# Optimization experiments

Hardware: AMD Instinct MI355X
Metric: run time of the kernel (lower is better)

The kernel has to match this reference:

```python
import jax, jax.numpy as jnp
import numpy as np

H = 1.0  # primo_h
N_GRID = 768


def _grid_mesh(n):
    ii, jj = np.meshgrid(np.arange(n - 1), np.arange(n - 1), indexing='ij')
    v00 = (ii * n + jj).ravel(); v10 = ((ii + 1) * n + jj).ravel()
    v01 = (ii * n + jj + 1).ravel(); v11 = ((ii + 1) * n + jj + 1).ravel()
    tri1 = np.stack([v00, v10, v01], 1); tri2 = np.stack([v10, v11, v01], 1)
    return np.concatenate([tri1, tri2], 0).astype(np.int32)  # [F,3]


def _face_adjacency(faces):
    # faces: [F,3] -> edges [E,2] (sorted vertex pairs), face_ids [E,2]
    F = faces.shape[0]
    fe = np.stack([faces[:, [0, 1]], faces[:, [1, 2]], faces[:, [2, 0]]], 1).reshape(-1, 2)
    fe = np.sort(fe, axis=1)
    fid = np.repeat(np.arange(F, dtype=np.int32), 3)
    order = np.lexsort((fe[:, 1], fe[:, 0]))
    fs, fi = fe[order], fid[order]
    same = np.all(fs[:-1] == fs[1:], axis=1)
    k = np.nonzero(same)[0]
    edges = fs[k].astype(np.int32)
    face_ids = np.stack([fi[k], fi[k + 1]], 1).astype(np.int32)
    return edges, face_ids


def setup_inputs() -> dict:
    key = jax.random.key(0)
    k1, k2, k3 = jax.random.split(key, 3)
    faces_np = _grid_mesh(N_GRID)                      # [F,3]
    edges_np, face_ids_np = _face_adjacency(faces_np)  # [E,2],[E,2]
    F = faces_np.shape[0]
    V = N_GRID * N_GRID
    return {
        'transformed_prism': jax.random.normal(k1, (F, 3, 3), dtype=jnp.float32),
        'rotations': jax.random.normal(k2, (F, 3, 3), dtype=jnp.float32),
        'verts': jax.random.normal(k3, (1, V, 3), dtype=jnp.float32),
        'faces': jnp.asarray(faces_np.T),       # [3,F], matches torch forward arg
        'edges': jnp.asarray(edges_np),
        'face_ids': jnp.asarray(face_ids_np),
    }


def _verts_id_face(Ft, E, Q):
    # Ft: [F,3] faces; E: [e,2] edge vertex ids; Q: [e,2] adjacent face ids
    fa, fb = Ft[Q[:, 0]], Ft[Q[:, 1]]  # [e,3]

    def find(fv, tgt):
        return jnp.where(fv[:, 0] == tgt, 0,
               jnp.where(fv[:, 1] == tgt, 1,
               jnp.where(fv[:, 2] == tgt, 2, -1)))

    return jnp.stack([find(fa, E[:, 0]), find(fa, E[:, 1]),
                      find(fb, E[:, 0]), find(fb, E[:, 1])], axis=1)  # [e,4]


def reference(transformed_prism, rotations, verts, faces, edges, face_ids):
    tp = transformed_prism
    bs = verts.shape[0]
    v = verts.reshape(-1, 3)
    Ft = faces.T  # [F,3]

    # per-face normals (vectorized version of the original per-face loop)
    e1 = tp[:, 0] - tp[:, 1]
    e2 = tp[:, 0] - tp[:, 2]
    nrm = jnp.cross(e1, e2)
    normals = nrm / jnp.linalg.norm(nrm, axis=-1, keepdims=True)  # [F,3]

    # face areas
    p1, p2, p3 = v[Ft[:, 0]], v[Ft[:, 1]], v[Ft[:, 2]]
    face_areas = 0.5 * jnp.linalg.norm(jnp.cross(p2 - p1, p3 - p1), axis=1)

    # faithful to original: normals indexed by edge VERTEX ids
    n1, n2 = normals[edges[:, 0]], normals[edges[:, 1]]
    fid1, fid2 = face_ids[:, 0], face_ids[:, 1]
    r1, r2 = rotations[fid1], rotations[fid2]

    ftv = _verts_id_face(Ft, edges, face_ids)  # [e,4]
    v1_p1, v2_p1 = tp[fid1, ftv[:, 0]], tp[fid1, ftv[:, 1]]
    v1_p2, v2_p2 = tp[fid2, ftv[:, 2]], tp[fid2, ftv[:, 3]]

    p1n1 = jnp.einsum('ec,ecd->ed', n1, r1)
    p1n2 = jnp.einsum('ec,ecd->ed', n2, r1)
    p2n1 = jnp.einsum('ec,ecd->ed', n1, r2)
    p2n2 = jnp.einsum('ec,ecd->ed', n2, r2)

    A = jnp.stack([v1_p1 + p1n1 * H, v2_p1 + p1n2 * H,
                   v1_p1 - p1n1 * H, v2_p1 - p1n2 * H], axis=1)  # [e,4,3]
    B = jnp.stack([v1_p2 + p2n1 * H, v2_p2 + p2n2 * H,
                   v1_p2 - p2n1 * H, v2_p2 - p2n2 * H], axis=1)
    D = A - B

    # coeff[p,q] = 2^{-|i_p-i_q|-|j_p-j_q|}, (i,j) over {0,1}^2
    idx = jnp.array([[0, 0], [0, 1], [1, 0], [1, 1]], dtype=jnp.float32)
    coeff = 2.0 ** (-jnp.abs(idx[:, None] - idx[None, :]).sum(-1))  # [4,4]
    pair = jnp.einsum('epc,eqc->epq', D, D)
    energy = (pair * coeff).sum((1, 2)) / 9.0  # [e]

    weight = jnp.sum((v[edges[:, 0]] - v[edges[:, 1]]) ** 2, axis=1) \
             / (face_areas[fid1] + face_areas[fid2])
    return (energy * weight).sum() / bs
```

## Files before the change

kernel.cpp:

```cpp
#include <hip/hip_runtime.h>


struct __attribute__((aligned(4))) F4 { float a, b, c, d; };
struct __attribute__((aligned(4))) F3 { float x, y, z; };

__device__ __forceinline__ void load9(const float* __restrict__ p, float* d) {
    F4 u0 = *(const F4*)p;
    F4 u1 = *(const F4*)(p + 4);
    d[0] = u0.a; d[1] = u0.b; d[2] = u0.c; d[3] = u0.d;
    d[4] = u1.a; d[5] = u1.b; d[6] = u1.c; d[7] = u1.d;
    d[8] = p[8];
}

__device__ __forceinline__ void load6(const float* __restrict__ p, float* d) {
    F4 u = *(const F4*)p;
    d[0] = u.a; d[1] = u.b; d[2] = u.c; d[3] = u.d;
    d[4] = p[4]; d[5] = p[5];
}

__device__ __forceinline__ F3 load3(const float* __restrict__ p) {
    F3 r; r.x = p[0]; r.y = p[1]; r.z = p[2]; return r;
}

__device__ __forceinline__ float edge_ew(const float* u1, const float* u2,
                                         const float* w1, const float* w2,
                                         const float* rA, const float* rB,
                                         const F3& n1, const F3& n2,
                                         const F3& pa, const F3& pb,
                                         float asum) {
    float ux = u1[0] - u2[0], uy = u1[1] - u2[1], uz = u1[2] - u2[2];
    float wx = w1[0] - w2[0], wy = w1[1] - w2[1], wz = w1[2] - w2[2];

    float d0 = rA[0] - rB[0], d1 = rA[1] - rB[1], d2 = rA[2] - rB[2];
    float d3 = rA[3] - rB[3], d4 = rA[4] - rB[4], d5 = rA[5] - rB[5];
    float d6 = rA[6] - rB[6], d7 = rA[7] - rB[7], d8 = rA[8] - rB[8];

    float ax = n1.x * d0 + n1.y * d3 + n1.z * d6;
    float ay = n1.x * d1 + n1.y * d4 + n1.z * d7;
    float az = n1.x * d2 + n1.y * d5 + n1.z * d8;
    float bx = n2.x * d0 + n2.y * d3 + n2.z * d6;
    float by = n2.x * d1 + n2.y * d4 + n2.z * d7;
    float bz = n2.x * d2 + n2.y * d5 + n2.z * d8;

    float uu = ux * ux + uy * uy + uz * uz;
    float ww = wx * wx + wy * wy + wz * wz;
    float uw = ux * wx + uy * wy + uz * wz;
    float aa = ax * ax + ay * ay + az * az;
    float bb = bx * bx + by * by + bz * bz;
    float ab = ax * bx + ay * by + az * bz;
    float energy = (3.0f * (uu + ww + uw) + (aa + bb + ab)) * (1.0f / 9.0f);

    float dx = pa.x - pb.x, dy = pa.y - pb.y, dz = pa.z - pb.z;
    float weight = (dx * dx + dy * dy + dz * dz) / asum;
    return energy * weight;
}

__global__ void prep_kernel(const float* __restrict__ tp,
                            const float* __restrict__ verts,
                            float* __restrict__ normals,
                            float* __restrict__ areas,
                            double* __restrict__ acc,
                            int n, int V, int Q) {
    int t = blockIdx.x * blockDim.x + threadIdx.x;
    if (t == 0) *acc = 0.0;

    if (t < V) {
        float r[9];
        load9(tp + (size_t)9 * t, r);
        float e1x = r[0] - r[3], e1y = r[1] - r[4], e1z = r[2] - r[5];
        float e2x = r[0] - r[6], e2y = r[1] - r[7], e2z = r[2] - r[8];
        float nx = e1y * e2z - e1z * e2y;
        float ny = e1z * e2x - e1x * e2z;
        float nz = e1x * e2y - e1y * e2x;
        float inv = 1.0f / sqrtf(nx * nx + ny * ny + nz * nz);
        normals[3 * t]     = nx * inv;
        normals[3 * t + 1] = ny * inv;
        normals[3 * t + 2] = nz * inv;
    }

    if (t < Q) {
        int m = n - 1;
        int i = t / m;
        int j = t - i * m;
        int v00 = i * n + j;
        F3 p00 = load3(verts + (size_t)3 * v00);
        F3 p01 = load3(verts + (size_t)3 * (v00 + 1));
        F3 p10 = load3(verts + (size_t)3 * (v00 + n));
        F3 p11 = load3(verts + (size_t)3 * (v00 + n + 1));
        {
            float ax = p10.x - p00.x, ay = p10.y - p00.y, az = p10.z - p00.z;
            float bx = p01.x - p00.x, by = p01.y - p00.y, bz = p01.z - p00.z;
            float cx = ay * bz - az * by;
            float cy = az * bx - ax * bz;
            float cz = ax * by - ay * bx;
            areas[t] = 0.5f * sqrtf(cx * cx + cy * cy + cz * cz);
        }
        {
            float ax = p11.x - p10.x, ay = p11.y - p10.y, az = p11.z - p10.z;
            float bx = p01.x - p10.x, by = p01.y - p10.y, bz = p01.z - p10.z;
            float cx = ay * bz - az * by;
            float cy = az * bx - ax * bz;
            float cz = ax * by - ay * bx;
            areas[Q + t] = 0.5f * sqrtf(cx * cx + cy * cy + cz * cz);
        }
    }
}

__global__ void edge_kernel(const float* __restrict__ tp,
                            const float* __restrict__ rot,
                            const float* __restrict__ verts,
                            const float* __restrict__ normals,
                            const float* __restrict__ areas,
                            double* __restrict__ acc,
                            int n, int Q) {
    int q = blockIdx.x * blockDim.x + threadIdx.x;
    double term = 0.0;
    if (q < Q) {
        int m = n - 1;
        int i = q / m;
        int j = q - i * m;
        int v00 = i * n + j;
        int v01 = v00 + 1;
        int v10 = v00 + n;

        float t1[9], t2[9], r1[9], r2[9];
        load9(tp  + (size_t)9 * q, t1);
        load9(tp  + (size_t)9 * (Q + q), t2);
        load9(rot + (size_t)9 * q, r1);
        load9(rot + (size_t)9 * (Q + q), r2);
        float a1 = areas[q];
        float a2 = areas[Q + q];

        F3 nA = load3(normals + (size_t)3 * v00);
        F3 nB = load3(normals + (size_t)3 * v01);
        F3 nC = load3(normals + (size_t)3 * v10);
        F3 pA = load3(verts + (size_t)3 * v00);
        F3 pB = load3(verts + (size_t)3 * v01);
        F3 pC = load3(verts + (size_t)3 * v10);

        float sum = 0.0f;
        sum += edge_ew(t1 + 6, t2 + 6, t1 + 3, t2 + 0, r1, r2,
                       nB, nC, pB, pC, a1 + a2);
        if (i > 0) {
            int f2 = Q + q - m;
            float rh[9], th[6];
            load9(rot + (size_t)9 * f2, rh);
            load6(tp + (size_t)9 * f2, th);
            sum += edge_ew(t1 + 0, th + 0, t1 + 6, th + 3, r1, rh,
                           nA, nB, pA, pB, a1 + areas[f2]);
        }
        if (j > 0) {
            int f2 = Q + q - 1;
            float rv[9], tv[6];
            load9(rot + (size_t)9 * f2, rv);
            load6(tp + (size_t)9 * f2 + 3, tv);
            sum += edge_ew(t1 + 0, tv + 3, t1 + 3, tv + 0, r1, rv,
                           nA, nC, pA, pC, a1 + areas[f2]);
        }
        term = (double)sum;
    }

#pragma unroll
    for (int off = 32; off > 0; off >>= 1) term += __shfl_down(term, off, 64);
    __shared__ double sdata[4];
    int lane = threadIdx.x & 63;
    int wid = threadIdx.x >> 6;
    if (lane == 0) sdata[wid] = term;
    __syncthreads();
    if (threadIdx.x == 0) {
        double s = sdata[0] + sdata[1] + sdata[2] + sdata[3];
        atomicAdd(acc, s);
    }
}

__global__ void finalize_kernel(const double* __restrict__ acc,
                                float* __restrict__ out) {
    if (threadIdx.x == 0 && blockIdx.x == 0) out[0] = (float)(*acc);
}

extern "C" void kernel_launch(void* const* d_in, const int* in_sizes, int n_in,
                              void* d_out, int out_size, void* d_ws, size_t ws_size,
                              hipStream_t stream) {
    const float* tp    = (const float*)d_in[0];
    const float* rot   = (const float*)d_in[1];
    const float* verts = (const float*)d_in[2];

    int V = in_sizes[2] / 3;
    int n = (int)(sqrtf((float)V) + 0.5f);
    int Q = (n - 1) * (n - 1);

    double* acc     = (double*)d_ws;
    float*  normals = (float*)((char*)d_ws + 16);
    float*  areas   = normals + (size_t)3 * V;
    float*  out     = (float*)d_out;

    const int B = 256;
    int gp = (max(V, Q) + B - 1) / B;
    prep_kernel<<<gp, B, 0, stream>>>(tp, verts, normals, areas, acc, n, V, Q);
    int ge = (Q + B - 1) / B;
    edge_kernel<<<ge, B, 0, stream>>>(tp, rot, verts, normals, areas, acc, n, Q);
    finalize_kernel<<<1, 64, 0, stream>>>(acc, out);
}
```

Before: 170.9 us.

## Fuse prep and edge kernels into a 2D-tiled kernel with shared-memory halos

Replaces the separate normals/areas prep kernel and per-quad edge kernel with one 2D-tiled kernel. Each block stages its faces, neighbor faces, vertices and recomputed normals and areas in LDS, including halos, so the intermediate arrays are never written to or read back from global memory. The global double atomic is replaced by per-block partials summed in a final reduction kernel. In exchange, halo data is loaded and recomputed redundantly, the stride-9 element-wise loads into LDS may coalesce poorly, and the large LDS footprint (roughly 40 KB per block) limits occupancy.

```diff
diff --git a/kernel.cpp b/kernel.cpp
--- a/kernel.cpp
+++ b/kernel.cpp
@@ -1,25 +1,22 @@
 #include <hip/hip_runtime.h>
 
 
-struct __attribute__((aligned(4))) F4 { float a, b, c, d; };
-struct __attribute__((aligned(4))) F3 { float x, y, z; };
+#define TI 8
+#define TJ 32
+
+struct __attribute__((aligned(4))) F4s { float a, b, c, d; };
+struct F3 { float x, y, z; };
 
 __device__ __forceinline__ void load9(const float* __restrict__ p, float* d) {
-    F4 u0 = *(const F4*)p;
-    F4 u1 = *(const F4*)(p + 4);
+    F4s u0 = *(const F4s*)p;
+    F4s u1 = *(const F4s*)(p + 4);
     d[0] = u0.a; d[1] = u0.b; d[2] = u0.c; d[3] = u0.d;
     d[4] = u1.a; d[5] = u1.b; d[6] = u1.c; d[7] = u1.d;
     d[8] = p[8];
 }
 
-__device__ __forceinline__ void load6(const float* __restrict__ p, float* d) {
-    F4 u = *(const F4*)p;
-    d[0] = u.a; d[1] = u.b; d[2] = u.c; d[3] = u.d;
-    d[4] = p[4]; d[5] = p[5];
-}
-
-__device__ __forceinline__ F3 load3(const float* __restrict__ p) {
-    F3 r; r.x = p[0]; r.y = p[1]; r.z = p[2]; return r;
+__device__ __forceinline__ int iclamp(int x, int lo, int hi) {
+    return x < lo ? lo : (x > hi ? hi : x);
 }
 
 __device__ __forceinline__ float edge_ew(const float* u1, const float* u2,
@@ -51,131 +48,165 @@
     float energy = (3.0f * (uu + ww + uw) + (aa + bb + ab)) * (1.0f / 9.0f);
 
     float dx = pa.x - pb.x, dy = pa.y - pb.y, dz = pa.z - pb.z;
-    float weight = (dx * dx + dy * dy + dz * dz) / asum;
-    return energy * weight;
-}
-
-__global__ void prep_kernel(const float* __restrict__ tp,
-                            const float* __restrict__ verts,
-                            float* __restrict__ normals,
-                            float* __restrict__ areas,
-                            double* __restrict__ acc,
-                            int n, int V, int Q) {
-    int t = blockIdx.x * blockDim.x + threadIdx.x;
-    if (t == 0) *acc = 0.0;
-
-    if (t < V) {
+    return energy * (dx * dx + dy * dy + dz * dz) / asum;
+}
+
+__global__ __launch_bounds__(256) void fused_kernel(
+        const float* __restrict__ tp,
+        const float* __restrict__ rot,
+        const float* __restrict__ verts,
+        double* __restrict__ partials,
+        int n) {
+    const int m = n - 1;
+    const int Q = m * m;
+    const int tid = threadIdx.x;
+    const int i0 = blockIdx.y * TI;
+    const int j0 = blockIdx.x * TJ;
+
+    __shared__ float sT1[TI * TJ * 9];
+    __shared__ float sR1[TI * TJ * 9];
+    __shared__ float sT2[(TI + 1) * (TJ + 1) * 9];
+    __shared__ float sR2[(TI + 1) * (TJ + 1) * 9];
+    __shared__ float sV[(TI + 2) * (TJ + 2) * 3];
+    __shared__ float sN[(TI + 1) * (TJ + 1) * 3];
+    __shared__ float sA1[TI * TJ];
+    __shared__ float sA2[(TI + 1) * (TJ + 1)];
+    __shared__ double sred[4];
+
+    for (int idx = tid; idx < TI * TJ * 9; idx += 256) {
+        int r = idx / (TJ * 9);
+        int o = idx - r * (TJ * 9);
+        int k = o / 9, c = o - k * 9;
+        int gi = iclamp(i0 + r, 0, m - 1);
+        int gj = iclamp(j0 + k, 0, m - 1);
+        size_t f = (size_t)gi * m + gj;
+        sT1[idx] = tp[9 * f + c];
+        sR1[idx] = rot[9 * f + c];
+    }
+    for (int idx = tid; idx < (TI + 1) * (TJ + 1) * 9; idx += 256) {
+        int r = idx / ((TJ + 1) * 9);
+        int o = idx - r * ((TJ + 1) * 9);
+        int k = o / 9, c = o - k * 9;
+        int gi = iclamp(i0 - 1 + r, 0, m - 1);
+        int gj = iclamp(j0 - 1 + k, 0, m - 1);
+        size_t f = (size_t)Q + (size_t)gi * m + gj;
+        sT2[idx] = tp[9 * f + c];
+        sR2[idx] = rot[9 * f + c];
+    }
+    for (int idx = tid; idx < (TI + 2) * (TJ + 2) * 3; idx += 256) {
+        int r = idx / ((TJ + 2) * 3);
+        int o = idx - r * ((TJ + 2) * 3);
+        int k = o / 3, c = o - k * 3;
+        int gi = iclamp(i0 - 1 + r, 0, n - 1);
+        int gj = iclamp(j0 - 1 + k, 0, n - 1);
+        sV[idx] = verts[3 * ((size_t)gi * n + gj) + c];
+    }
+    for (int v = tid; v < (TI + 1) * (TJ + 1); v += 256) {
+        int vi = v / (TJ + 1), vj = v - vi * (TJ + 1);
+        int gi = iclamp(i0 + vi, 0, n - 1);
+        int gj = iclamp(j0 + vj, 0, n - 1);
         float r[9];
-        load9(tp + (size_t)9 * t, r);
+        load9(tp + 9 * ((size_t)gi * n + gj), r);
         float e1x = r[0] - r[3], e1y = r[1] - r[4], e1z = r[2] - r[5];
         float e2x = r[0] - r[6], e2y = r[1] - r[7], e2z = r[2] - r[8];
         float nx = e1y * e2z - e1z * e2y;
         float ny = e1z * e2x - e1x * e2z;
         float nz = e1x * e2y - e1y * e2x;
         float inv = 1.0f / sqrtf(nx * nx + ny * ny + nz * nz);
-        normals[3 * t]     = nx * inv;
-        normals[3 * t + 1] = ny * inv;
-        normals[3 * t + 2] = nz * inv;
-    }
-
-    if (t < Q) {
-        int m = n - 1;
-        int i = t / m;
-        int j = t - i * m;
-        int v00 = i * n + j;
-        F3 p00 = load3(verts + (size_t)3 * v00);
-        F3 p01 = load3(verts + (size_t)3 * (v00 + 1));
-        F3 p10 = load3(verts + (size_t)3 * (v00 + n));
-        F3 p11 = load3(verts + (size_t)3 * (v00 + n + 1));
-        {
-            float ax = p10.x - p00.x, ay = p10.y - p00.y, az = p10.z - p00.z;
-            float bx = p01.x - p00.x, by = p01.y - p00.y, bz = p01.z - p00.z;
-            float cx = ay * bz - az * by;
-            float cy = az * bx - ax * bz;
-            float cz = ax * by - ay * bx;
-            areas[t] = 0.5f * sqrtf(cx * cx + cy * cy + cz * cz);
-        }
-        {
-            float ax = p11.x - p10.x, ay = p11.y - p10.y, az = p11.z - p10.z;
-            float bx = p01.x - p10.x, by = p01.y - p10.y, bz = p01.z - p10.z;
-            float cx = ay * bz - az * by;
-            float cy = az * bx - ax * bz;
-            float cz = ax * by - ay * bx;
-            areas[Q + t] = 0.5f * sqrtf(cx * cx + cy * cy + cz * cz);
-        }
-    }
-}
-
-__global__ void edge_kernel(const float* __restrict__ tp,
-                            const float* __restrict__ rot,
-                            const float* __restrict__ verts,
-                            const float* __restrict__ normals,
-                            const float* __restrict__ areas,
-                            double* __restrict__ acc,
-                            int n, int Q) {
-    int q = blockIdx.x * blockDim.x + threadIdx.x;
+        sN[3 * v] = nx * inv; sN[3 * v + 1] = ny * inv; sN[3 * v + 2] = nz * inv;
+    }
+
+    __syncthreads();
+
+    {
+        int ti = tid / TJ, tj = tid - ti * TJ;
+        const float* p00 = sV + 3 * ((ti + 1) * (TJ + 2) + (tj + 1));
+        const float* p10 = sV + 3 * ((ti + 2) * (TJ + 2) + (tj + 1));
+        const float* p01 = sV + 3 * ((ti + 1) * (TJ + 2) + (tj + 2));
+        float ax = p10[0] - p00[0], ay = p10[1] - p00[1], az = p10[2] - p00[2];
+        float bx = p01[0] - p00[0], by = p01[1] - p00[1], bz = p01[2] - p00[2];
+        float cx = ay * bz - az * by, cy = az * bx - ax * bz, cz = ax * by - ay * bx;
+        sA1[tid] = 0.5f * sqrtf(cx * cx + cy * cy + cz * cz);
+    }
+    for (int v = tid; v < (TI + 1) * (TJ + 1); v += 256) {
+        int r = v / (TJ + 1), k = v - r * (TJ + 1);
+        const float* p10 = sV + 3 * ((r + 1) * (TJ + 2) + k);
+        const float* p11 = sV + 3 * ((r + 1) * (TJ + 2) + (k + 1));
+        const float* p01 = sV + 3 * (r * (TJ + 2) + (k + 1));
+        float ax = p11[0] - p10[0], ay = p11[1] - p10[1], az = p11[2] - p10[2];
+        float bx = p01[0] - p10[0], by = p01[1] - p10[1], bz = p01[2] - p10[2];
+        float cx = ay * bz - az * by, cy = az * bx - ax * bz, cz = ax * by - ay * bx;
+        sA2[v] = 0.5f * sqrtf(cx * cx + cy * cy + cz * cz);
+    }
+
+    __syncthreads();
+
+    int ti = tid / TJ, tj = tid - ti * TJ;
+    int i = i0 + ti, j = j0 + tj;
     double term = 0.0;
-    if (q < Q) {
-        int m = n - 1;
-        int i = q / m;
-        int j = q - i * m;
-        int v00 = i * n + j;
-        int v01 = v00 + 1;
-        int v10 = v00 + n;
-
-        float t1[9], t2[9], r1[9], r2[9];
-        load9(tp  + (size_t)9 * q, t1);
-        load9(tp  + (size_t)9 * (Q + q), t2);
-        load9(rot + (size_t)9 * q, r1);
-        load9(rot + (size_t)9 * (Q + q), r2);
-        float a1 = areas[q];
-        float a2 = areas[Q + q];
-
-        F3 nA = load3(normals + (size_t)3 * v00);
-        F3 nB = load3(normals + (size_t)3 * v01);
-        F3 nC = load3(normals + (size_t)3 * v10);
-        F3 pA = load3(verts + (size_t)3 * v00);
-        F3 pB = load3(verts + (size_t)3 * v01);
-        F3 pC = load3(verts + (size_t)3 * v10);
+    if (i < m && j < m) {
+        const float* t1 = sT1 + 9 * tid;
+        const float* r1 = sR1 + 9 * tid;
+        const float* t2c = sT2 + 9 * ((ti + 1) * (TJ + 1) + (tj + 1));
+        const float* r2c = sR2 + 9 * ((ti + 1) * (TJ + 1) + (tj + 1));
+        float a1 = sA1[tid];
+
+        F3 nA = { sN[3 * (ti * (TJ + 1) + tj)],
+                  sN[3 * (ti * (TJ + 1) + tj) + 1],
+                  sN[3 * (ti * (TJ + 1) + tj) + 2] };
+        F3 nB = { sN[3 * (ti * (TJ + 1) + tj + 1)],
+                  sN[3 * (ti * (TJ + 1) + tj + 1) + 1],
+                  sN[3 * (ti * (TJ + 1) + tj + 1) + 2] };
+        F3 nC = { sN[3 * ((ti + 1) * (TJ + 1) + tj)],
+                  sN[3 * ((ti + 1) * (TJ + 1) + tj) + 1],
+                  sN[3 * ((ti + 1) * (TJ + 1) + tj) + 2] };
+        const float* pv00 = sV + 3 * ((ti + 1) * (TJ + 2) + (tj + 1));
+        const float* pv01 = sV + 3 * ((ti + 1) * (TJ + 2) + (tj + 2));
+        const float* pv10 = sV + 3 * ((ti + 2) * (TJ + 2) + (tj + 1));
+        F3 pA = { pv00[0], pv00[1], pv00[2] };
+        F3 pB = { pv01[0], pv01[1], pv01[2] };
+        F3 pC = { pv10[0], pv10[1], pv10[2] };
 
         float sum = 0.0f;
-        sum += edge_ew(t1 + 6, t2 + 6, t1 + 3, t2 + 0, r1, r2,
-                       nB, nC, pB, pC, a1 + a2);
+        sum += edge_ew(t1 + 6, t2c + 6, t1 + 3, t2c + 0, r1, r2c,
+                       nB, nC, pB, pC, a1 + sA2[(ti + 1) * (TJ + 1) + (tj + 1)]);
         if (i > 0) {
-            int f2 = Q + q - m;
-            float rh[9], th[6];
-            load9(rot + (size_t)9 * f2, rh);
-            load6(tp + (size_t)9 * f2, th);
+            const float* th = sT2 + 9 * (ti * (TJ + 1) + (tj + 1));
+            const float* rh = sR2 + 9 * (ti * (TJ + 1) + (tj + 1));
             sum += edge_ew(t1 + 0, th + 0, t1 + 6, th + 3, r1, rh,
-                           nA, nB, pA, pB, a1 + areas[f2]);
+                           nA, nB, pA, pB, a1 + sA2[ti * (TJ + 1) + (tj + 1)]);
         }
         if (j > 0) {
-            int f2 = Q + q - 1;
-            float rv[9], tv[6];
-            load9(rot + (size_t)9 * f2, rv);
-            load6(tp + (size_t)9 * f2 + 3, tv);
-            sum += edge_ew(t1 + 0, tv + 3, t1 + 3, tv + 0, r1, rv,
-                           nA, nC, pA, pC, a1 + areas[f2]);
+            const float* tv = sT2 + 9 * ((ti + 1) * (TJ + 1) + tj);
+            const float* rv = sR2 + 9 * ((ti + 1) * (TJ + 1) + tj);
+            sum += edge_ew(t1 + 0, tv + 6, t1 + 3, tv + 3, r1, rv,
+                           nA, nC, pA, pC, a1 + sA2[(ti + 1) * (TJ + 1) + tj]);
         }
         term = (double)sum;
     }
 
 #pragma unroll
     for (int off = 32; off > 0; off >>= 1) term += __shfl_down(term, off, 64);
-    __shared__ double sdata[4];
-    int lane = threadIdx.x & 63;
-    int wid = threadIdx.x >> 6;
-    if (lane == 0) sdata[wid] = term;
-    __syncthreads();
-    if (threadIdx.x == 0) {
-        double s = sdata[0] + sdata[1] + sdata[2] + sdata[3];
-        atomicAdd(acc, s);
-    }
-}
-
-__global__ void finalize_kernel(const double* __restrict__ acc,
-                                float* __restrict__ out) {
-    if (threadIdx.x == 0 && blockIdx.x == 0) out[0] = (float)(*acc);
+    int lane = tid & 63, wid = tid >> 6;
+    if (lane == 0) sred[wid] = term;
+    __syncthreads();
+    if (tid == 0) {
+        partials[blockIdx.y * gridDim.x + blockIdx.x] =
+            sred[0] + sred[1] + sred[2] + sred[3];
+    }
+}
+
+__global__ __launch_bounds__(256) void finalize_kernel(
+        const double* __restrict__ partials, int P, float* __restrict__ out) {
+    double s = 0.0;
+    for (int i = threadIdx.x; i < P; i += 256) s += partials[i];
+#pragma unroll
+    for (int off = 32; off > 0; off >>= 1) s += __shfl_down(s, off, 64);
+    __shared__ double sred[4];
+    int lane = threadIdx.x & 63, wid = threadIdx.x >> 6;
+    if (lane == 0) sred[wid] = s;
+    __syncthreads();
+    if (threadIdx.x == 0) out[0] = (float)(sred[0] + sred[1] + sred[2] + sred[3]);
 }
 
 extern "C" void kernel_launch(void* const* d_in, const int* in_sizes, int n_in,
@@ -187,17 +218,13 @@
 
     int V = in_sizes[2] / 3;
     int n = (int)(sqrtf((float)V) + 0.5f);
-    int Q = (n - 1) * (n - 1);
-
-    double* acc     = (double*)d_ws;
-    float*  normals = (float*)((char*)d_ws + 16);
-    float*  areas   = normals + (size_t)3 * V;
-    float*  out     = (float*)d_out;
-
-    const int B = 256;
-    int gp = (max(V, Q) + B - 1) / B;
-    prep_kernel<<<gp, B, 0, stream>>>(tp, verts, normals, areas, acc, n, V, Q);
-    int ge = (Q + B - 1) / B;
-    edge_kernel<<<ge, B, 0, stream>>>(tp, rot, verts, normals, areas, acc, n, Q);
-    finalize_kernel<<<1, 64, 0, stream>>>(acc, out);
-}
+    int m = n - 1;
+
+    double* partials = (double*)d_ws;
+    float*  out      = (float*)d_out;
+
+    dim3 grid((m + TJ - 1) / TJ, (m + TI - 1) / TI);
+    int P = grid.x * grid.y;
+    fused_kernel<<<grid, 256, 0, stream>>>(tp, rot, verts, partials, n);
+    finalize_kernel<<<1, 256, 0, stream>>>(partials, P, out);
+}
```

Measured after the change: 180.7 us. +5.8%, slower.
